# Kernel tuning notes

Measured on AMD Instinct MI355X. Metric: run time of the kernel, lower is better.

The kernel has to match this reference:

```python
import jax, jax.numpy as jnp
import numpy as np

NU = 20000; NI = 20000; E = 200000; H = 8; D = 64; F = H * D
B = 1024; P = 8; K = 8


def gat(h, W, al, ar, b, src, dst, N):
    # DGL GATConv (eval mode, dropout off): fc -> edge attention -> edge softmax -> scatter-sum -> bias -> elu
    f = (h @ W).reshape(N, H, D)                       # [N,H,D]
    el = jnp.einsum('nhd,hd->nh', f, al)               # [N,H]
    er = jnp.einsum('nhd,hd->nh', f, ar)
    e = jax.nn.leaky_relu(el[src] + er[dst], 0.2)      # [E,H]
    m = jax.ops.segment_max(e, dst, num_segments=N)    # [N,H]
    m = jnp.where(jnp.isfinite(m), m, 0.0)             # nodes w/ zero in-degree
    ex = jnp.exp(e - m[dst])                           # [E,H]
    s = jax.ops.segment_sum(ex, dst, num_segments=N)   # [N,H]
    alpha = ex / jnp.maximum(s[dst], 1e-9)             # [E,H]
    out = jax.ops.segment_sum(alpha[:, :, None] * f[src], dst, num_segments=N)  # [N,H,D]
    return jax.nn.elu(out.reshape(N, F) + b)


def semantic_attention(z, W1, b1, v):
    # z: [N, M, F]
    w = jnp.mean(jnp.tanh(z @ W1 + b1) @ v, axis=0)    # [M]
    beta = jax.nn.softmax(w)
    return jnp.einsum('m,nmf->nf', beta, z)


def han_layer(h, Wg, al, ar, bg, W1, b1, v, src, dst, N):
    zs = [gat(h, Wg[i], al[i], ar[i], bg[i], src[i], dst[i], N) for i in range(Wg.shape[0])]
    return semantic_attention(jnp.stack(zs, axis=1), W1, b1, v)


def setup_inputs() -> dict:
    key = jax.random.key(0)
    ks = jax.random.split(key, 24)
    sc = 0.05
    return {
        'user_embs': jax.random.normal(ks[0], (NU, D), jnp.float32) * sc,
        'item_embs': jax.random.normal(ks[1], (NI, D), jnp.float32) * sc,
        'Wg_u': jax.random.normal(ks[2], (2, D, F), jnp.float32) * sc,
        'al_u': jax.random.normal(ks[3], (2, H, D), jnp.float32) * sc,
        'ar_u': jax.random.normal(ks[4], (2, H, D), jnp.float32) * sc,
        'bg_u': jax.random.normal(ks[5], (2, F), jnp.float32) * sc,
        'Ws_u': jax.random.normal(ks[6], (F, 128), jnp.float32) * sc,
        'bs_u': jax.random.normal(ks[7], (128,), jnp.float32) * sc,
        'vs_u': jax.random.normal(ks[8], (128,), jnp.float32) * sc,
        'Wg_i': jax.random.normal(ks[9], (2, D, F), jnp.float32) * sc,
        'al_i': jax.random.normal(ks[10], (2, H, D), jnp.float32) * sc,
        'ar_i': jax.random.normal(ks[11], (2, H, D), jnp.float32) * sc,
        'bg_i': jax.random.normal(ks[12], (2, F), jnp.float32) * sc,
        'Ws_i': jax.random.normal(ks[13], (F, 128), jnp.float32) * sc,
        'bs_i': jax.random.normal(ks[14], (128,), jnp.float32) * sc,
        'vs_i': jax.random.normal(ks[15], (128,), jnp.float32) * sc,
        'src_u': jax.random.randint(ks[16], (2, E), 0, NU, jnp.int32),
        'dst_u': jax.random.randint(ks[17], (2, E), 0, NU, jnp.int32),
        'src_i': jax.random.randint(ks[18], (2, E), 0, NI, jnp.int32),
        'dst_i': jax.random.randint(ks[19], (2, E), 0, NI, jnp.int32),
        'uid': jax.random.randint(ks[20], (B,), 0, NU, jnp.int32),
        'pos': jax.random.randint(ks[21], (B, P), 0, NI, jnp.int32),
        'neg': jax.random.randint(ks[22], (B, P, K), 0, NI, jnp.int32),
    }


def reference(user_embs, item_embs, Wg_u, al_u, ar_u, bg_u, Ws_u, bs_u, vs_u,
              Wg_i, al_i, ar_i, bg_i, Ws_i, bs_i, vs_i,
              src_u, dst_u, src_i, dst_i, uid, pos, neg):
    hu = han_layer(user_embs, Wg_u, al_u, ar_u, bg_u, Ws_u, bs_u, vs_u, src_u, dst_u, NU)  # [NU,F]
    hi = han_layer(item_embs, Wg_i, al_i, ar_i, bg_i, Ws_i, bs_i, vs_i, src_i, dst_i, NI)  # [NI,F]
    ue = hu[uid]                                     # [B,F]
    pe = hi[pos]                                     # [B,P,F]
    ne = hi[neg]                                     # [B,P,K,F]
    ue_p = jnp.broadcast_to(ue[:, None, :], pe.shape)
    pos_logits = (ue_p * pe).sum(-1)[..., None]      # [B,P,1]
    ue_n = jnp.broadcast_to(ue_p[:, :, None, :], ne.shape)
    neg_logits = (ue_n * ne).sum(-1)                 # [B,P,K]
    return pos_logits, neg_logits, ue_n, pe, ne
```

## Files before the change

kernel.cpp:

```cpp
#include <hip/hip_runtime.h>
#include <hip/hip_bf16.h>
#include <cstddef>

#define NN 20000
#define EE 200000

typedef __attribute__((ext_vector_type(8))) short bf8_t;
typedef __attribute__((ext_vector_type(4))) float f32x4;

__device__ __forceinline__ float bf2f(unsigned int lo16) {
    return __uint_as_float(lo16 << 16);
}
__device__ __forceinline__ float hi16f(unsigned int u) {
    return __uint_as_float(u & 0xffff0000u);
}
__device__ __forceinline__ unsigned short f2bf(float f) {
    unsigned u = __float_as_uint(f);
    u += 0x7fffu + ((u >> 16) & 1u);
    return (unsigned short)(u >> 16);
}

__global__ void prep_kernel(
    const float* __restrict__ user_embs, const float* __restrict__ item_embs,
    const float* __restrict__ Wg_u, const float* __restrict__ Wg_i,
    const float* __restrict__ Ws_u, const float* __restrict__ Ws_i,
    unsigned short* __restrict__ hb,
    unsigned short* __restrict__ Wt,
    unsigned short* __restrict__ W1t,
    int* __restrict__ count, int* __restrict__ cursor,
    float* __restrict__ wsum)
{
    int i = blockIdx.x * 256 + threadIdx.x;
    if (i < 2 * NN * 64) {
        float v = (i < NN * 64) ? user_embs[i] : item_embs[i - NN * 64];
        hb[i] = f2bf(v);
    }
    if (i < 4 * 512 * 64) {
        int tg = i >> 15, rem = i & 32767;
        int col = rem >> 6, k = rem & 63;
        const float* W = (tg < 2 ? Wg_u + tg * 32768 : Wg_i + (tg - 2) * 32768);
        Wt[i] = f2bf(W[k * 512 + col]);
    }
    if (i < 2 * 128 * 512) {
        int t = i >> 16, rem = i & 65535;
        int c = rem >> 9, k = rem & 511;
        const float* Wsrc = t ? Ws_i : Ws_u;
        W1t[i] = f2bf(Wsrc[k * 128 + c]);
    }
    if (i < 4 * NN) { count[i] = 0; cursor[i] = 0; }
    if (i < 4) wsum[i] = 0.f;
}

__global__ __launch_bounds__(256) void fc_kernel(
    const unsigned short* __restrict__ hb,
    const unsigned short* __restrict__ Wt,
    const float* __restrict__ al_u, const float* __restrict__ ar_u,
    const float* __restrict__ al_i, const float* __restrict__ ar_i,
    unsigned short* __restrict__ fb,
    float* __restrict__ el, float* __restrict__ er)
{
    const int tg = blockIdx.y, t = tg >> 1, g = tg & 1;
    const int tid = threadIdx.x, wid = tid >> 6, lane = tid & 63;
    const int r0 = blockIdx.x * 16;
    const unsigned short* A = hb + (size_t)t * NN * 64;
    const unsigned short* B = Wt + (size_t)tg * 512 * 64;
    const float* alf = (t ? al_i : al_u) + g * 512;
    const float* arf = (t ? ar_i : ar_u) + g * 512;

    const int arow = lane & 15, ak0 = (lane >> 4) * 8;
    const bf8_t a0 = *(const bf8_t*)(A + (size_t)(r0 + arow) * 64 + ak0);
    const bf8_t a1 = *(const bf8_t*)(A + (size_t)(r0 + arow) * 64 + 32 + ak0);

    f32x4 acc[8];
#pragma unroll
    for (int i = 0; i < 8; ++i) acc[i] = f32x4{0.f, 0.f, 0.f, 0.f};

#pragma unroll
    for (int tn = 0; tn < 8; ++tn) {
        const unsigned short* bp =
            B + (size_t)(wid * 128 + tn * 16 + (lane & 15)) * 64 + ak0;
        bf8_t b0 = *(const bf8_t*)(bp);
        bf8_t b1 = *(const bf8_t*)(bp + 32);
        acc[tn] = __builtin_amdgcn_mfma_f32_16x16x32_bf16(a0, b0, acc[tn], 0, 0, 0);
        acc[tn] = __builtin_amdgcn_mfma_f32_16x16x32_bf16(a1, b1, acc[tn], 0, 0, 0);
    }

    float elp[2][4], erp[2][4];
#pragma unroll
    for (int hs = 0; hs < 2; ++hs)
#pragma unroll
        for (int r = 0; r < 4; ++r) { elp[hs][r] = 0.f; erp[hs][r] = 0.f; }

#pragma unroll
    for (int tn = 0; tn < 8; ++tn) {
        const int hs = tn >> 2;
        const int col = wid * 128 + tn * 16 + (lane & 15);
        const float av = alf[col], rv = arf[col];
#pragma unroll
        for (int r = 0; r < 4; ++r) {
            elp[hs][r] += acc[tn][r] * av;
            erp[hs][r] += acc[tn][r] * rv;
        }
    }
#pragma unroll
    for (int m = 1; m < 16; m <<= 1) {
#pragma unroll
        for (int hs = 0; hs < 2; ++hs)
#pragma unroll
            for (int r = 0; r < 4; ++r) {
                elp[hs][r] += __shfl_xor(elp[hs][r], m, 64);
                erp[hs][r] += __shfl_xor(erp[hs][r], m, 64);
            }
    }
    if ((lane & 15) == 0) {
        float* elg = el + (size_t)tg * NN * 8;
        float* erg = er + (size_t)tg * NN * 8;
#pragma unroll
        for (int r = 0; r < 4; ++r) {
            const int n = r0 + (lane >> 4) * 4 + r;
            elg[n * 8 + 2 * wid + 0] = elp[0][r];
            elg[n * 8 + 2 * wid + 1] = elp[1][r];
            erg[n * 8 + 2 * wid + 0] = erp[0][r];
            erg[n * 8 + 2 * wid + 1] = erp[1][r];
        }
    }

    __shared__ unsigned short sf[16][512];
#pragma unroll
    for (int tn = 0; tn < 8; ++tn)
#pragma unroll
        for (int r = 0; r < 4; ++r)
            sf[(lane >> 4) * 4 + r][wid * 128 + tn * 16 + (lane & 15)] =
                f2bf(acc[tn][r]);
    __syncthreads();
    unsigned short* fo = fb + (size_t)tg * NN * 512;
#pragma unroll
    for (int s = 0; s < 4; ++s) {
        int ch = tid + s * 256;
        int row = ch >> 6, off = (ch & 63) * 8;
        *(uint4*)(fo + (size_t)(r0 + row) * 512 + off) = *(uint4*)&sf[row][off];
    }
}

__global__ void hist_kernel(const int* __restrict__ dst_u,
                            const int* __restrict__ dst_i,
                            int* __restrict__ count)
{
    int g = blockIdx.y;
    int i = blockIdx.x * 256 + threadIdx.x;
    if (i < EE) {
        const int* d = (g < 2 ? dst_u : dst_i) + (size_t)(g & 1) * EE;
        atomicAdd(&count[g * NN + d[i]], 1);
    }
}

__global__ __launch_bounds__(256) void scan1_kernel(
    const int* __restrict__ count, int* __restrict__ tmp,
    int* __restrict__ partials)
{
    const int g = blockIdx.y, tid = threadIdx.x;
    const int i = blockIdx.x * 256 + tid;
    __shared__ int sc[256];
    int v = (i < NN) ? count[g * NN + i] : 0;
    sc[tid] = v;
    __syncthreads();
#pragma unroll
    for (int off = 1; off < 256; off <<= 1) {
        int add = (tid >= off) ? sc[tid - off] : 0;
        __syncthreads();
        sc[tid] += add;
        __syncthreads();
    }
    if (i < NN) tmp[g * NN + i] = sc[tid] - v;
    if (tid == 255) partials[g * 79 + blockIdx.x] = sc[255];
}

__global__ __launch_bounds__(256) void scan2_kernel(
    const int* __restrict__ partials, int* __restrict__ bases)
{
    __shared__ int p[320], bl[320];
    const int tid = threadIdx.x;
    for (int i = tid; i < 316; i += 256) p[i] = partials[i];
    __syncthreads();
    if (tid < 4) {
        int base = 0;
        for (int b = 0; b < 79; ++b) { bl[tid * 79 + b] = base; base += p[tid * 79 + b]; }
    }
    __syncthreads();
    for (int i = tid; i < 316; i += 256) bases[i] = bl[i];
}

__global__ void scan3_kernel(const int* __restrict__ tmp,
                             const int* __restrict__ bases,
                             int* __restrict__ roff)
{
    const int g = blockIdx.y;
    const int i = blockIdx.x * 256 + threadIdx.x;
    if (i < NN) roff[g * (NN + 1) + i] = tmp[g * NN + i] + bases[g * 79 + blockIdx.x];
    if (blockIdx.x == 0 && threadIdx.x == 0) roff[g * (NN + 1) + NN] = EE;
}

__global__ void scatter_kernel(const int* __restrict__ src_u,
                               const int* __restrict__ dst_u,
                               const int* __restrict__ src_i,
                               const int* __restrict__ dst_i,
                               const int* __restrict__ roff,
                               int* __restrict__ cursor,
                               int* __restrict__ csrc)
{
    int g = blockIdx.y;
    int i = blockIdx.x * 256 + threadIdx.x;
    if (i < EE) {
        const int* s = (g < 2 ? src_u : src_i) + (size_t)(g & 1) * EE;
        const int* d = (g < 2 ? dst_u : dst_i) + (size_t)(g & 1) * EE;
        int dd = d[i];
        int pp = atomicAdd(&cursor[g * NN + dd], 1);
        csrc[(size_t)g * EE + roff[g * (NN + 1) + dd] + pp] = s[i];
    }
}

__global__ __launch_bounds__(256) void agg_kernel(
    const unsigned short* __restrict__ fb,
    const float* __restrict__ el, const float* __restrict__ er,
    const int* __restrict__ roff, const int* __restrict__ csrc,
    const float* __restrict__ bg_u, const float* __restrict__ bg_i,
    unsigned short* __restrict__ zb)
{
    const int tg = blockIdx.y, t = tg >> 1, g = tg & 1;
    const int tid = threadIdx.x, wid = tid >> 6, lane = tid & 63;
    const int n = blockIdx.x * 4 + wid;
    const unsigned short* fg = fb + (size_t)tg * NN * 512;
    const float* elg = el + (size_t)tg * NN * 8;
    const float* erg = er + (size_t)tg * NN * 8;
    const int* ro = roff + (size_t)tg * (NN + 1);
    const int* cs = csrc + (size_t)tg * EE;
    const float* bias = (t ? bg_i : bg_u) + g * 512;

    const int h = lane >> 3, c0 = lane * 8;
    const float ern = erg[n * 8 + h];
    const int beg = ro[n], end = ro[n + 1];

    float s = 0.f;
    float a0 = 0.f, a1 = 0.f, a2 = 0.f, a3 = 0.f, a4 = 0.f, a5 = 0.f, a6 = 0.f, a7 = 0.f;
    for (int e = beg; e < end; ++e) {
        int src = cs[e];
        float x = elg[src * 8 + h] + ern;
        x = (x >= 0.f) ? x : 0.2f * x;
        float ex = __expf(x);
        s += ex;
        uint4 fv = *(const uint4*)(fg + (size_t)src * 512 + c0);
        a0 += ex * bf2f(fv.x & 0xffffu);  a1 += ex * hi16f(fv.x);
        a2 += ex * bf2f(fv.y & 0xffffu);  a3 += ex * hi16f(fv.y);
        a4 += ex * bf2f(fv.z & 0xffffu);  a5 += ex * hi16f(fv.z);
        a6 += ex * bf2f(fv.w & 0xffffu);  a7 += ex * hi16f(fv.w);
    }
    const float inv = 1.f / fmaxf(s, 1e-9f);
    const float4 bA = *(const float4*)(bias + c0);
    const float4 bB = *(const float4*)(bias + c0 + 4);
    float o0 = a0 * inv + bA.x; o0 = o0 > 0.f ? o0 : expm1f(o0);
    float o1 = a1 * inv + bA.y; o1 = o1 > 0.f ? o1 : expm1f(o1);
    float o2 = a2 * inv + bA.z; o2 = o2 > 0.f ? o2 : expm1f(o2);
    float o3 = a3 * inv + bA.w; o3 = o3 > 0.f ? o3 : expm1f(o3);
    float o4 = a4 * inv + bB.x; o4 = o4 > 0.f ? o4 : expm1f(o4);
    float o5 = a5 * inv + bB.y; o5 = o5 > 0.f ? o5 : expm1f(o5);
    float o6 = a6 * inv + bB.z; o6 = o6 > 0.f ? o6 : expm1f(o6);
    float o7 = a7 * inv + bB.w; o7 = o7 > 0.f ? o7 : expm1f(o7);
    uint4 pk;
    pk.x = ((unsigned)f2bf(o1) << 16) | f2bf(o0);
    pk.y = ((unsigned)f2bf(o3) << 16) | f2bf(o2);
    pk.z = ((unsigned)f2bf(o5) << 16) | f2bf(o4);
    pk.w = ((unsigned)f2bf(o7) << 16) | f2bf(o6);
    *(uint4*)(zb + (size_t)tg * NN * 512 + (size_t)n * 512 + c0) = pk;
}

__global__ __launch_bounds__(256) void sem_kernel(
    const unsigned short* __restrict__ zb,
    const unsigned short* __restrict__ W1t,
    const float* __restrict__ bs_u, const float* __restrict__ vs_u,
    const float* __restrict__ bs_i, const float* __restrict__ vs_i,
    float* __restrict__ wsum)
{
    const int tm = blockIdx.y, t = tm >> 1;
    const int tid = threadIdx.x, wid = tid >> 6, lane = tid & 63;
    const int r0 = blockIdx.x * 32;
    const unsigned short* Az = zb + (size_t)tm * NN * 512;
    const unsigned short* Bw = W1t + (size_t)t * 128 * 512;
    const float* b1f = t ? bs_i : bs_u;
    const float* vf  = t ? vs_i : vs_u;

    const int arow = lane & 15, ak0 = (lane >> 4) * 8;
    const int col0 = wid * 32 + (lane & 15);
    const unsigned short* a0p = Az + (size_t)(r0 + arow) * 512 + ak0;
    const unsigned short* a1p = a0p + 16 * 512;
    const unsigned short* b0p = Bw + (size_t)col0 * 512 + ak0;
    const unsigned short* b1p = b0p + 16 * 512;

    f32x4 acc00 = f32x4{0.f,0.f,0.f,0.f}, acc01 = acc00, acc10 = acc00, acc11 = acc00;
#pragma unroll 4
    for (int k = 0; k < 512; k += 32) {
        bf8_t a0 = *(const bf8_t*)(a0p + k);
        bf8_t a1 = *(const bf8_t*)(a1p + k);
        bf8_t b0 = *(const bf8_t*)(b0p + k);
        bf8_t b1 = *(const bf8_t*)(b1p + k);
        acc00 = __builtin_amdgcn_mfma_f32_16x16x32_bf16(a0, b0, acc00, 0, 0, 0);
        acc01 = __builtin_amdgcn_mfma_f32_16x16x32_bf16(a0, b1, acc01, 0, 0, 0);
        acc10 = __builtin_amdgcn_mfma_f32_16x16x32_bf16(a1, b0, acc10, 0, 0, 0);
        acc11 = __builtin_amdgcn_mfma_f32_16x16x32_bf16(a1, b1, acc11, 0, 0, 0);
    }

    const float b1c0 = b1f[col0], b1c1 = b1f[col0 + 16];
    const float vc0 = vf[col0],  vc1 = vf[col0 + 16];
    float q = 0.f;
#pragma unroll
    for (int r = 0; r < 4; ++r) {
        q += tanhf(acc00[r] + b1c0) * vc0;
        q += tanhf(acc01[r] + b1c1) * vc1;
        q += tanhf(acc10[r] + b1c0) * vc0;
        q += tanhf(acc11[r] + b1c1) * vc1;
    }
#pragma unroll
    for (int m = 1; m < 64; m <<= 1) q += __shfl_xor(q, m, 64);
    __shared__ float red[4];
    if (lane == 0) red[wid] = q;
    __syncthreads();
    if (tid == 0) atomicAdd(&wsum[tm], red[0] + red[1] + red[2] + red[3]);
}

__device__ __forceinline__ void comb8(uint4 q0, uint4 q1, float b0, float b1,
                                      float* __restrict__ o)
{
    o[0] = b0 * bf2f(q0.x & 0xffffu) + b1 * bf2f(q1.x & 0xffffu);
    o[1] = b0 * hi16f(q0.x)          + b1 * hi16f(q1.x);
    o[2] = b0 * bf2f(q0.y & 0xffffu) + b1 * bf2f(q1.y & 0xffffu);
    o[3] = b0 * hi16f(q0.y)          + b1 * hi16f(q1.y);
    o[4] = b0 * bf2f(q0.z & 0xffffu) + b1 * bf2f(q1.z & 0xffffu);
    o[5] = b0 * hi16f(q0.z)          + b1 * hi16f(q1.z);
    o[6] = b0 * bf2f(q0.w & 0xffffu) + b1 * bf2f(q1.w & 0xffffu);
    o[7] = b0 * hi16f(q0.w)          + b1 * hi16f(q1.w);
}

__global__ __launch_bounds__(64) void score_kernel(
    const unsigned short* __restrict__ zb,
    const float* __restrict__ wsum,
    const int* __restrict__ uid, const int* __restrict__ pos,
    const int* __restrict__ neg, float* __restrict__ out)
{
    const int bp = blockIdx.x, b = bp >> 3;
    const int lane = threadIdx.x;
    const int c0 = lane * 8;

    const float wu0 = wsum[0] * (1.f / (float)NN), wu1 = wsum[1] * (1.f / (float)NN);
    const float mu = fmaxf(wu0, wu1);
    const float eu0 = __expf(wu0 - mu), eu1 = __expf(wu1 - mu);
    const float su = 1.f / (eu0 + eu1);
    const float bu0 = eu0 * su, bu1 = eu1 * su;
    const float wi0 = wsum[2] * (1.f / (float)NN), wi1 = wsum[3] * (1.f / (float)NN);
    const float mi = fmaxf(wi0, wi1);
    const float ei0 = __expf(wi0 - mi), ei1 = __expf(wi1 - mi);
    const float si = 1.f / (ei0 + ei1);
    const float bi0 = ei0 * si, bi1 = ei1 * si;

    const unsigned short* zu0 = zb;
    const unsigned short* zu1 = zb + (size_t)NN * 512;
    const unsigned short* zi0 = zb + (size_t)2 * NN * 512;
    const unsigned short* zi1 = zb + (size_t)3 * NN * 512;

    float* pos_logits = out;
    float* neg_logits = out + 8192;
    float* ue_n       = out + 73728;
    float* pe         = out + 33628160;
    float* ne         = out + 37822464;

    float u[8];
    {
        const size_t off = (size_t)uid[b] * 512 + c0;
        comb8(*(const uint4*)(zu0 + off), *(const uint4*)(zu1 + off), bu0, bu1, u);
    }

    {
        const size_t off = (size_t)pos[bp] * 512 + c0;
        float pv[8];
        comb8(*(const uint4*)(zi0 + off), *(const uint4*)(zi1 + off), bi0, bi1, pv);
        float* pr = pe + (size_t)bp * 512 + c0;
        *(float4*)(pr)     = make_float4(pv[0], pv[1], pv[2], pv[3]);
        *(float4*)(pr + 4) = make_float4(pv[4], pv[5], pv[6], pv[7]);
        float d = u[0]*pv[0] + u[1]*pv[1] + u[2]*pv[2] + u[3]*pv[3]
                + u[4]*pv[4] + u[5]*pv[5] + u[6]*pv[6] + u[7]*pv[7];
#pragma unroll
        for (int off2 = 32; off2; off2 >>= 1) d += __shfl_down(d, off2, 64);
        if (lane == 0) pos_logits[bp] = d;
    }

    for (int k = 0; k < 8; ++k) {
        const size_t row = (size_t)bp * 8 + k;
        const size_t off = (size_t)neg[row] * 512 + c0;
        float nv[8];
        comb8(*(const uint4*)(zi0 + off), *(const uint4*)(zi1 + off), bi0, bi1, nv);
        float* nr = ne + row * 512 + c0;
        *(float4*)(nr)     = make_float4(nv[0], nv[1], nv[2], nv[3]);
        *(float4*)(nr + 4) = make_float4(nv[4], nv[5], nv[6], nv[7]);
        float* ur = ue_n + row * 512 + c0;
        *(float4*)(ur)     = make_float4(u[0], u[1], u[2], u[3]);
        *(float4*)(ur + 4) = make_float4(u[4], u[5], u[6], u[7]);
        float d = u[0]*nv[0] + u[1]*nv[1] + u[2]*nv[2] + u[3]*nv[3]
                + u[4]*nv[4] + u[5]*nv[5] + u[6]*nv[6] + u[7]*nv[7];
#pragma unroll
        for (int off2 = 32; off2; off2 >>= 1) d += __shfl_down(d, off2, 64);
        if (lane == 0) neg_logits[row] = d;
    }
}

extern "C" void kernel_launch(void* const* d_in, const int* in_sizes, int n_in,
                              void* d_out, int out_size, void* d_ws, size_t ws_size,
                              hipStream_t stream)
{
    const float* user_embs = (const float*)d_in[0];
    const float* item_embs = (const float*)d_in[1];
    const float* Wg_u = (const float*)d_in[2];
    const float* al_u = (const float*)d_in[3];
    const float* ar_u = (const float*)d_in[4];
    const float* bg_u = (const float*)d_in[5];
    const float* Ws_u = (const float*)d_in[6];
    const float* bs_u = (const float*)d_in[7];
    const float* vs_u = (const float*)d_in[8];
    const float* Wg_i = (const float*)d_in[9];
    const float* al_i = (const float*)d_in[10];
    const float* ar_i = (const float*)d_in[11];
    const float* bg_i = (const float*)d_in[12];
    const float* Ws_i = (const float*)d_in[13];
    const float* bs_i = (const float*)d_in[14];
    const float* vs_i = (const float*)d_in[15];
    const int* src_u = (const int*)d_in[16];
    const int* dst_u = (const int*)d_in[17];
    const int* src_i = (const int*)d_in[18];
    const int* dst_i = (const int*)d_in[19];
    const int* uid = (const int*)d_in[20];
    const int* pos = (const int*)d_in[21];
    const int* neg = (const int*)d_in[22];

    char* p = (char*)d_ws;
    auto carve = [&](size_t bytes) {
        char* r = p; p += (bytes + 255) & ~(size_t)255; return r;
    };
    unsigned short* fb  = (unsigned short*)carve((size_t)4 * NN * 512 * 2);
    unsigned short* zb  = (unsigned short*)carve((size_t)4 * NN * 512 * 2);
    unsigned short* hb  = (unsigned short*)carve((size_t)2 * NN * 64 * 2);
    unsigned short* Wt  = (unsigned short*)carve((size_t)4 * 512 * 64 * 2);
    unsigned short* W1t = (unsigned short*)carve((size_t)2 * 128 * 512 * 2);
    float* el   = (float*)carve((size_t)4 * NN * 8 * 4);
    float* er   = (float*)carve((size_t)4 * NN * 8 * 4);
    float* wsum = (float*)carve(64);
    int* count    = (int*)carve((size_t)4 * NN * 4);
    int* cursor   = (int*)carve((size_t)4 * NN * 4);
    int* tmp      = (int*)carve((size_t)4 * NN * 4);
    int* roff     = (int*)carve((size_t)4 * (NN + 1) * 4);
    int* partials = (int*)carve(320 * 4);
    int* bases    = (int*)carve(320 * 4);
    int* csrc     = (int*)carve((size_t)4 * EE * 4);

    prep_kernel<<<(2 * NN * 64 + 255) / 256, 256, 0, stream>>>(
        user_embs, item_embs, Wg_u, Wg_i, Ws_u, Ws_i, hb, Wt, W1t,
        count, cursor, wsum);
    hist_kernel<<<dim3((EE + 255) / 256, 4), 256, 0, stream>>>(dst_u, dst_i, count);
    scan1_kernel<<<dim3(79, 4), 256, 0, stream>>>(count, tmp, partials);
    scan2_kernel<<<1, 256, 0, stream>>>(partials, bases);
    scan3_kernel<<<dim3(79, 4), 256, 0, stream>>>(tmp, bases, roff);
    scatter_kernel<<<dim3((EE + 255) / 256, 4), 256, 0, stream>>>(
        src_u, dst_u, src_i, dst_i, roff, cursor, csrc);
    fc_kernel<<<dim3(NN / 16, 4), 256, 0, stream>>>(
        hb, Wt, al_u, ar_u, al_i, ar_i, fb, el, er);
    agg_kernel<<<dim3(NN / 4, 4), 256, 0, stream>>>(
        fb, el, er, roff, csrc, bg_u, bg_i, zb);
    sem_kernel<<<dim3(NN / 32, 4), 256, 0, stream>>>(
        zb, W1t, bs_u, vs_u, bs_i, vs_i, wsum);
    score_kernel<<<1024 * 8, 64, 0, stream>>>(zb, wsum, uid, pos, neg, (float*)d_out);
}
```

Measured before the change: 691.8 us.

## Merge three-pass scan into one kernel and fuse scatter with fc launch

Replaces the three-kernel exclusive scan (block scan, partial scan, add bases) with a single 1024-thread block per graph. Each thread serially scans 20 counts and the block then does a shared-memory scan. The CSR scatter is also folded into the fc kernel as extra leading blocks, so the two independent stages share one launch. This removes three launches and the temp/partials buffers. The trade-off is a single-block scan with a serial 20-element loop per thread and heterogeneous blocks in one grid.

```diff
diff --git a/kernel.cpp b/kernel.cpp
--- a/kernel.cpp
+++ b/kernel.cpp
@@ -51,7 +51,55 @@
     if (i < 4) wsum[i] = 0.f;
 }
 
-__global__ __launch_bounds__(256) void fc_kernel(
+__global__ void hist_kernel(const int* __restrict__ dst_u,
+                            const int* __restrict__ dst_i,
+                            int* __restrict__ count)
+{
+    int g = blockIdx.y;
+    int i = blockIdx.x * 256 + threadIdx.x;
+    if (i < EE) {
+        const int* d = (g < 2 ? dst_u : dst_i) + (size_t)(g & 1) * EE;
+        atomicAdd(&count[g * NN + d[i]], 1);
+    }
+}
+
+__global__ __launch_bounds__(1024) void scan_kernel(
+    const int* __restrict__ count, int* __restrict__ roff)
+{
+    const int g = blockIdx.x, tid = threadIdx.x;
+    __shared__ int sc[1024];
+    int loc[20];
+    int s = 0;
+    const int base = tid * 20;
+#pragma unroll
+    for (int j = 0; j < 20; ++j) {
+        int idx = base + j;
+        int v = (idx < NN) ? count[g * NN + idx] : 0;
+        loc[j] = s;
+        s += v;
+    }
+    sc[tid] = s;
+    __syncthreads();
+    for (int off = 1; off < 1024; off <<= 1) {
+        int add = (tid >= off) ? sc[tid - off] : 0;
+        __syncthreads();
+        sc[tid] += add;
+        __syncthreads();
+    }
+    const int myoff = tid ? sc[tid - 1] : 0;
+#pragma unroll
+    for (int j = 0; j < 20; ++j) {
+        int idx = base + j;
+        if (idx < NN) roff[g * (NN + 1) + idx] = myoff + loc[j];
+    }
+    if (tid == 1023) roff[g * (NN + 1) + NN] = sc[1023];
+}
+
+__global__ __launch_bounds__(256) void scatter_fc_kernel(
+    const int* __restrict__ src_u, const int* __restrict__ dst_u,
+    const int* __restrict__ src_i, const int* __restrict__ dst_i,
+    const int* __restrict__ roff, int* __restrict__ cursor,
+    int* __restrict__ csrc,
     const unsigned short* __restrict__ hb,
     const unsigned short* __restrict__ Wt,
     const float* __restrict__ al_u, const float* __restrict__ ar_u,
@@ -59,9 +107,24 @@
     unsigned short* __restrict__ fb,
     float* __restrict__ el, float* __restrict__ er)
 {
+    __shared__ unsigned short sf[16][512];
+
+    if (blockIdx.x < 782) {
+        int g = blockIdx.y;
+        int i = blockIdx.x * 256 + threadIdx.x;
+        if (i < EE) {
+            const int* s = (g < 2 ? src_u : src_i) + (size_t)(g & 1) * EE;
+            const int* d = (g < 2 ? dst_u : dst_i) + (size_t)(g & 1) * EE;
+            int dd = d[i];
+            int pp = atomicAdd(&cursor[g * NN + dd], 1);
+            csrc[(size_t)g * EE + roff[g * (NN + 1) + dd] + pp] = s[i];
+        }
+        return;
+    }
+
     const int tg = blockIdx.y, t = tg >> 1, g = tg & 1;
     const int tid = threadIdx.x, wid = tid >> 6, lane = tid & 63;
-    const int r0 = blockIdx.x * 16;
+    const int r0 = (blockIdx.x - 782) * 16;
     const unsigned short* A = hb + (size_t)t * NN * 64;
     const unsigned short* B = Wt + (size_t)tg * 512 * 64;
     const float* alf = (t ? al_i : al_u) + g * 512;
@@ -125,7 +188,6 @@
         }
     }
 
-    __shared__ unsigned short sf[16][512];
 #pragma unroll
     for (int tn = 0; tn < 8; ++tn)
 #pragma unroll
@@ -139,83 +201,6 @@
         int ch = tid + s * 256;
         int row = ch >> 6, off = (ch & 63) * 8;
         *(uint4*)(fo + (size_t)(r0 + row) * 512 + off) = *(uint4*)&sf[row][off];
-    }
-}
-
-__global__ void hist_kernel(const int* __restrict__ dst_u,
-                            const int* __restrict__ dst_i,
-                            int* __restrict__ count)
-{
-    int g = blockIdx.y;
-    int i = blockIdx.x * 256 + threadIdx.x;
-    if (i < EE) {
-        const int* d = (g < 2 ? dst_u : dst_i) + (size_t)(g & 1) * EE;
-        atomicAdd(&count[g * NN + d[i]], 1);
-    }
-}
-
-__global__ __launch_bounds__(256) void scan1_kernel(
-    const int* __restrict__ count, int* __restrict__ tmp,
-    int* __restrict__ partials)
-{
-    const int g = blockIdx.y, tid = threadIdx.x;
-    const int i = blockIdx.x * 256 + tid;
-    __shared__ int sc[256];
-    int v = (i < NN) ? count[g * NN + i] : 0;
-    sc[tid] = v;
-    __syncthreads();
-#pragma unroll
-    for (int off = 1; off < 256; off <<= 1) {
-        int add = (tid >= off) ? sc[tid - off] : 0;
-        __syncthreads();
-        sc[tid] += add;
-        __syncthreads();
-    }
-    if (i < NN) tmp[g * NN + i] = sc[tid] - v;
-    if (tid == 255) partials[g * 79 + blockIdx.x] = sc[255];
-}
-
-__global__ __launch_bounds__(256) void scan2_kernel(
-    const int* __restrict__ partials, int* __restrict__ bases)
-{
-    __shared__ int p[320], bl[320];
-    const int tid = threadIdx.x;
-    for (int i = tid; i < 316; i += 256) p[i] = partials[i];
-    __syncthreads();
-    if (tid < 4) {
-        int base = 0;
-        for (int b = 0; b < 79; ++b) { bl[tid * 79 + b] = base; base += p[tid * 79 + b]; }
-    }
-    __syncthreads();
-    for (int i = tid; i < 316; i += 256) bases[i] = bl[i];
-}
-
-__global__ void scan3_kernel(const int* __restrict__ tmp,
-                             const int* __restrict__ bases,
-                             int* __restrict__ roff)
-{
-    const int g = blockIdx.y;
-    const int i = blockIdx.x * 256 + threadIdx.x;
-    if (i < NN) roff[g * (NN + 1) + i] = tmp[g * NN + i] + bases[g * 79 + blockIdx.x];
-    if (blockIdx.x == 0 && threadIdx.x == 0) roff[g * (NN + 1) + NN] = EE;
-}
-
-__global__ void scatter_kernel(const int* __restrict__ src_u,
-                               const int* __restrict__ dst_u,
-                               const int* __restrict__ src_i,
-                               const int* __restrict__ dst_i,
-                               const int* __restrict__ roff,
-                               int* __restrict__ cursor,
-                               int* __restrict__ csrc)
-{
-    int g = blockIdx.y;
-    int i = blockIdx.x * 256 + threadIdx.x;
-    if (i < EE) {
-        const int* s = (g < 2 ? src_u : src_i) + (size_t)(g & 1) * EE;
-        const int* d = (g < 2 ? dst_u : dst_i) + (size_t)(g & 1) * EE;
-        int dd = d[i];
-        int pp = atomicAdd(&cursor[g * NN + dd], 1);
-        csrc[(size_t)g * EE + roff[g * (NN + 1) + dd] + pp] = s[i];
     }
 }
 
@@ -450,24 +435,18 @@
     float* el   = (float*)carve((size_t)4 * NN * 8 * 4);
     float* er   = (float*)carve((size_t)4 * NN * 8 * 4);
     float* wsum = (float*)carve(64);
-    int* count    = (int*)carve((size_t)4 * NN * 4);
-    int* cursor   = (int*)carve((size_t)4 * NN * 4);
-    int* tmp      = (int*)carve((size_t)4 * NN * 4);
-    int* roff     = (int*)carve((size_t)4 * (NN + 1) * 4);
-    int* partials = (int*)carve(320 * 4);
-    int* bases    = (int*)carve(320 * 4);
-    int* csrc     = (int*)carve((size_t)4 * EE * 4);
+    int* count  = (int*)carve((size_t)4 * NN * 4);
+    int* cursor = (int*)carve((size_t)4 * NN * 4);
+    int* roff   = (int*)carve((size_t)4 * (NN + 1) * 4);
+    int* csrc   = (int*)carve((size_t)4 * EE * 4);
 
     prep_kernel<<<(2 * NN * 64 + 255) / 256, 256, 0, stream>>>(
         user_embs, item_embs, Wg_u, Wg_i, Ws_u, Ws_i, hb, Wt, W1t,
         count, cursor, wsum);
     hist_kernel<<<dim3((EE + 255) / 256, 4), 256, 0, stream>>>(dst_u, dst_i, count);
-    scan1_kernel<<<dim3(79, 4), 256, 0, stream>>>(count, tmp, partials);
-    scan2_kernel<<<1, 256, 0, stream>>>(partials, bases);
-    scan3_kernel<<<dim3(79, 4), 256, 0, stream>>>(tmp, bases, roff);
-    scatter_kernel<<<dim3((EE + 255) / 256, 4), 256, 0, stream>>>(
-        src_u, dst_u, src_i, dst_i, roff, cursor, csrc);
-    fc_kernel<<<dim3(NN / 16, 4), 256, 0, stream>>>(
+    scan_kernel<<<4, 1024, 0, stream>>>(count, roff);
+    scatter_fc_kernel<<<dim3(782 + NN / 16, 4), 256, 0, stream>>>(
+        src_u, dst_u, src_i, dst_i, roff, cursor, csrc,
         hb, Wt, al_u, ar_u, al_i, ar_i, fb, el, er);
     agg_kernel<<<dim3(NN / 4, 4), 256, 0, stream>>>(
         fb, el, er, roff, csrc, bg_u, bg_i, zb);
```

Result: no change. 690.0 us (-0.3%).
